# Optimization experiments

Measured on AMD Instinct MI355X. Metric: run time of the kernel, lower is better.

The kernel has to match this reference:

```python
import jax, jax.numpy as jnp
import numpy as np

B, S, D_MODEL, N_HEADS, D_K, D_V = 4, 1024, 1024, 16, 64, 64


def setup_inputs() -> dict:
    key = jax.random.key(0)
    ks = jax.random.split(key, 6)
    # xavier-normal std for [d_model, n_heads*d_k] weight
    std = float(np.sqrt(2.0 / (D_MODEL + N_HEADS * D_K)))
    return {
        "q": jax.random.normal(ks[0], (B, S, D_MODEL), jnp.float32),
        "k": jax.random.normal(ks[1], (B, S, D_MODEL), jnp.float32),
        "v": jax.random.normal(ks[2], (B, S, D_MODEL), jnp.float32),
        "w_q": jax.random.normal(ks[3], (D_MODEL, N_HEADS * D_K), jnp.float32) * std,
        "w_k": jax.random.normal(ks[4], (D_MODEL, N_HEADS * D_K), jnp.float32) * std,
        "w_v": jax.random.normal(ks[5], (D_MODEL, N_HEADS * D_V), jnp.float32) * std,
        "b_q": jnp.zeros((N_HEADS * D_K,), jnp.float32),
        "b_k": jnp.zeros((N_HEADS * D_K,), jnp.float32),
        "b_v": jnp.zeros((N_HEADS * D_V,), jnp.float32),
        "attn_mask": 0,  # falsy -> no masking, matching `if attn_mask:` in source
    }


def reference(q, k, v, w_q, w_k, w_v, b_q, b_k, b_v, attn_mask):
    b = q.shape[0]
    scale = jnp.sqrt(jnp.float32(D_K))
    # QKV projections -> [b, heads, seq, d]
    q_s = (q @ w_q + b_q).reshape(b, -1, N_HEADS, D_K).transpose(0, 2, 1, 3)
    k_s = (k @ w_k + b_k).reshape(b, -1, N_HEADS, D_K).transpose(0, 2, 1, 3)
    v_s = (v @ w_v + b_v).reshape(b, -1, N_HEADS, D_V).transpose(0, 2, 1, 3)
    scores = jnp.einsum("bhqd,bhkd->bhqk", q_s, k_s) / scale
    attn = jax.nn.softmax(scores, axis=-1)
    context = jnp.einsum("bhqk,bhkd->bhqd", attn, v_s)
    context = context.transpose(0, 2, 1, 3).reshape(b, -1, N_HEADS * D_V)
    return context, attn
```

## Files before the change

kernel.cpp:

```cpp
#include <hip/hip_runtime.h>

typedef unsigned short u16;
typedef __bf16 bf16x8 __attribute__((ext_vector_type(8)));
typedef float f32x4 __attribute__((ext_vector_type(4)));

__device__ __forceinline__ u16 f2b(float f) {
  unsigned u = __float_as_uint(f);
  return (u16)((u + 0x7FFFu + ((u >> 16) & 1u)) >> 16);
}
__device__ __forceinline__ float bl(unsigned w) { return __uint_as_float(w << 16); }
__device__ __forceinline__ float bh(unsigned w) { return __uint_as_float(w & 0xFFFF0000u); }

__device__ __forceinline__ void lds_load16(const void* g, void* l) {
  __builtin_amdgcn_global_load_lds(
      (__attribute__((address_space(1))) void*)(void*)g,
      (__attribute__((address_space(3))) void*)l, 16, 0, 0);
}

__global__ __launch_bounds__(256) void cvt_qkv(
    const float4* __restrict__ q, const float4* __restrict__ k, const float4* __restrict__ v,
    u16* __restrict__ qb, u16* __restrict__ kb, u16* __restrict__ vb) {
  int idx = blockIdx.x * 256 + threadIdx.x;
  int which = idx >> 20;
  int i = idx & 0xFFFFF;
  const float4* src = which == 0 ? q : which == 1 ? k : v;
  u16* dst = which == 0 ? qb : which == 1 ? kb : vb;
  float4 f = src[i];
  ushort4 o;
  o.x = f2b(f.x); o.y = f2b(f.y); o.z = f2b(f.z); o.w = f2b(f.w);
  *(ushort4*)(dst + (size_t)i * 4) = o;
}

__global__ __launch_bounds__(256) void transpose_cvt(
    const float* __restrict__ wq, const float* __restrict__ wk, const float* __restrict__ wv,
    u16* __restrict__ oq, u16* __restrict__ ok, u16* __restrict__ ov) {
  __shared__ float tile[32][33];
  int z = blockIdx.z;
  const float* in = z == 0 ? wq : z == 1 ? wk : wv;
  u16* out = z == 0 ? oq : z == 1 ? ok : ov;
  int x = blockIdx.x * 32 + threadIdx.x;
  for (int i = 0; i < 32; i += 8) {
    int y = blockIdx.y * 32 + threadIdx.y + i;
    tile[threadIdx.y + i][threadIdx.x] = in[(size_t)y * 1024 + x];
  }
  __syncthreads();
  int x2 = blockIdx.y * 32 + threadIdx.x;
  for (int i = 0; i < 32; i += 8) {
    int y2 = blockIdx.x * 32 + threadIdx.y + i;
    out[(size_t)y2 * 1024 + x2] = f2b(tile[threadIdx.x][threadIdx.y + i]);
  }
}

__global__ __launch_bounds__(256) void proj_gemm(
    const u16* __restrict__ qb, const u16* __restrict__ kb, const u16* __restrict__ vb,
    const u16* __restrict__ wqT, const u16* __restrict__ wkT, const u16* __restrict__ wvT,
    const float* __restrict__ bq, const float* __restrict__ bk, const float* __restrict__ bv,
    u16* __restrict__ q_s, u16* __restrict__ k_s, u16* __restrict__ vT_s) {
  __shared__ __align__(16) u16 As[128 * 64];
  __shared__ __align__(16) u16 Bs[128 * 64];
  const int z = blockIdx.z;
  const u16* A = z == 0 ? qb : z == 1 ? kb : vb;
  const u16* W = z == 0 ? wqT : z == 1 ? wkT : wvT;
  const float* bias = z == 0 ? bq : z == 1 ? bk : bv;

  const int t = threadIdx.x, lane = t & 63, wave = t >> 6;
  const int m0 = blockIdx.y * 128, n0 = blockIdx.x * 128;
  const int wm = (wave >> 1) * 64, wn = (wave & 1) * 64;

  f32x4 acc[4][4] = {};

  for (int k0 = 0; k0 < 1024; k0 += 64) {
    __syncthreads();
    #pragma unroll
    for (int r = 0; r < 4; ++r) {
      int flat = t + r * 256;
      int row = flat >> 3, gidx = (flat & 7) ^ (row & 7);
      lds_load16(A + (size_t)(m0 + row) * 1024 + k0 + gidx * 8, As + (size_t)flat * 8);
    }
    #pragma unroll
    for (int r = 0; r < 4; ++r) {
      int flat = t + r * 256;
      int row = flat >> 3, gidx = (flat & 7) ^ (row & 7);
      lds_load16(W + (size_t)(n0 + row) * 1024 + k0 + gidx * 8, Bs + (size_t)flat * 8);
    }
    __syncthreads();
    #pragma unroll
    for (int ks = 0; ks < 2; ++ks) {
      int kg = ks * 4 + (lane >> 4);
      bf16x8 af[4], bf[4];
      #pragma unroll
      for (int mi = 0; mi < 4; ++mi) {
        int rm = wm + mi * 16 + (lane & 15);
        af[mi] = *(const bf16x8*)(As + rm * 64 + ((kg ^ (rm & 7)) * 8));
      }
      #pragma unroll
      for (int ni = 0; ni < 4; ++ni) {
        int rn = wn + ni * 16 + (lane & 15);
        bf[ni] = *(const bf16x8*)(Bs + rn * 64 + ((kg ^ (rn & 7)) * 8));
      }
      #pragma unroll
      for (int mi = 0; mi < 4; ++mi)
        #pragma unroll
        for (int ni = 0; ni < 4; ++ni)
          acc[mi][ni] = __builtin_amdgcn_mfma_f32_16x16x32_bf16(af[mi], bf[ni], acc[mi][ni], 0, 0, 0);
    }
  }

  const float scale = (z == 0) ? 0.125f : 1.0f;
  #pragma unroll
  for (int mi = 0; mi < 4; ++mi) {
    #pragma unroll
    for (int ni = 0; ni < 4; ++ni) {
      int colb = n0 + wn + ni * 16 + (lane & 15);
      float bsv = bias[colb];
      int rowb0 = m0 + wm + mi * 16 + (lane >> 4) * 4;
      if (z == 2) {
        int bb = rowb0 >> 10, s0 = rowb0 & 1023;
        int hh = colb >> 6, dd = colb & 63;
        ushort4 o;
        o.x = f2b(acc[mi][ni][0] + bsv); o.y = f2b(acc[mi][ni][1] + bsv);
        o.z = f2b(acc[mi][ni][2] + bsv); o.w = f2b(acc[mi][ni][3] + bsv);
        *(ushort4*)(vT_s + ((((size_t)bb * 16 + hh) * 64 + dd) << 10) + s0) = o;
      } else {
        u16* dst = (z == 0) ? q_s : k_s;
        #pragma unroll
        for (int r = 0; r < 4; ++r)
          dst[(size_t)(rowb0 + r) * 1024 + colb] = f2b((acc[mi][ni][r] + bsv) * scale);
      }
    }
  }
}

#define SP_OFF   0
#define QT_OFF   132096
#define KV_OFF   140288
#define RED_OFF  156672
#define INV_OFF  158720
#define ATTN_LDS 158976

__global__ __launch_bounds__(512) void attn_kernel(
    const u16* __restrict__ q_s, const u16* __restrict__ k_s,
    const u16* __restrict__ vT_s, float* __restrict__ out_ctx,
    float* __restrict__ out_attn) {
  extern __shared__ __align__(16) char smem[];
  u16* s_p = (u16*)(smem + SP_OFF);
  u16* qt  = (u16*)(smem + QT_OFF);
  u16* kv  = (u16*)(smem + KV_OFF);
  float* red = (float*)(smem + RED_OFF);
  float* inv = (float*)(smem + INV_OFF);

  const int t = threadIdx.x, lane = t & 63, wave = t >> 6;
  const int mt = blockIdx.x, h = blockIdx.y, b = blockIdx.z;
  const int m0 = mt * 64;

  {
    int row = t >> 3, gidx = (t & 7) ^ (row & 7);
    lds_load16(q_s + ((size_t)(b * 1024 + m0 + row) * 1024 + h * 64 + gidx * 8),
               qt + (size_t)t * 8);
  }

  const int p1_mt = wave & 3;
  const int p1_nb = (wave >> 2) * 4;
  for (int c = 0; c < 8; ++c) {
    const int n0 = c * 128;
    __syncthreads();
    #pragma unroll
    for (int r = 0; r < 2; ++r) {
      int flat = t + r * 512;
      int row = flat >> 3, gidx = (flat & 7) ^ (row & 7);
      lds_load16(k_s + ((size_t)(b * 1024 + n0 + row) * 1024 + h * 64 + gidx * 8),
                 kv + (size_t)flat * 8);
    }
    __syncthreads();
    f32x4 acc[4] = {};
    #pragma unroll
    for (int ks = 0; ks < 2; ++ks) {
      int kg = ks * 4 + (lane >> 4);
      int am = p1_mt * 16 + (lane & 15);
      bf16x8 af = *(const bf16x8*)(qt + am * 64 + ((kg ^ (am & 7)) * 8));
      #pragma unroll
      for (int ni = 0; ni < 4; ++ni) {
        int bn = (p1_nb + ni) * 16 + (lane & 15);
        bf16x8 bf = *(const bf16x8*)(kv + bn * 64 + ((kg ^ (bn & 7)) * 8));
        acc[ni] = __builtin_amdgcn_mfma_f32_16x16x32_bf16(af, bf, acc[ni], 0, 0, 0);
      }
    }
    #pragma unroll
    for (int ni = 0; ni < 4; ++ni) {
      int col = n0 + (p1_nb + ni) * 16 + (lane & 15);
      int rbase = p1_mt * 16 + (lane >> 4) * 4;
      #pragma unroll
      for (int r = 0; r < 4; ++r) s_p[(rbase + r) * 1032 + col] = f2b(acc[ni][r]);
    }
  }

  __syncthreads();
  const int srow = t >> 3, sseg = t & 7;
  u16* rp = s_p + srow * 1032 + sseg * 128;
  float mx = -3.0e38f;
  #pragma unroll
  for (int i = 0; i < 16; ++i) {
    uint4 pk = *(const uint4*)(rp + i * 8);
    mx = fmaxf(mx, fmaxf(fmaxf(bl(pk.x), bh(pk.x)), fmaxf(bl(pk.y), bh(pk.y))));
    mx = fmaxf(mx, fmaxf(fmaxf(bl(pk.z), bh(pk.z)), fmaxf(bl(pk.w), bh(pk.w))));
  }
  red[t] = mx;
  __syncthreads();
  float rmx = red[srow * 8];
  #pragma unroll
  for (int j = 1; j < 8; ++j) rmx = fmaxf(rmx, red[srow * 8 + j]);
  __syncthreads();
  float sum = 0.f;
  #pragma unroll
  for (int i = 0; i < 16; ++i) {
    uint4 pk = *(const uint4*)(rp + i * 8);
    float e0 = __expf(bl(pk.x) - rmx), e1 = __expf(bh(pk.x) - rmx);
    float e2 = __expf(bl(pk.y) - rmx), e3 = __expf(bh(pk.y) - rmx);
    float e4 = __expf(bl(pk.z) - rmx), e5 = __expf(bh(pk.z) - rmx);
    float e6 = __expf(bl(pk.w) - rmx), e7 = __expf(bh(pk.w) - rmx);
    sum += ((e0 + e1) + (e2 + e3)) + ((e4 + e5) + (e6 + e7));
    pk.x = (unsigned)f2b(e0) | ((unsigned)f2b(e1) << 16);
    pk.y = (unsigned)f2b(e2) | ((unsigned)f2b(e3) << 16);
    pk.z = (unsigned)f2b(e4) | ((unsigned)f2b(e5) << 16);
    pk.w = (unsigned)f2b(e6) | ((unsigned)f2b(e7) << 16);
    *(uint4*)(rp + i * 8) = pk;
  }
  red[t] = sum;
  __syncthreads();
  float rs = 0.f;
  #pragma unroll
  for (int j = 0; j < 8; ++j) rs += red[srow * 8 + j];
  if (sseg == 0) inv[srow] = 1.0f / rs;
  __syncthreads();

  const size_t attn_base = ((size_t)(b * 16 + h) * 1024 + m0) << 10;
  #pragma unroll 4
  for (int it = 0; it < 32; ++it) {
    int flat = it * 512 + t;
    int r2 = flat >> 8, c4 = (flat & 255) << 2;
    float is = inv[r2];
    uint2 pk = *(const uint2*)(s_p + r2 * 1032 + c4);
    float4 o;
    o.x = bl(pk.x) * is; o.y = bh(pk.x) * is; o.z = bl(pk.y) * is; o.w = bh(pk.y) * is;
    *(float4*)(out_attn + attn_base + ((size_t)r2 << 10) + c4) = o;
  }

  const int p2_mt = wave >> 1;
  const int p2_nb = (wave & 1) * 2;
  f32x4 acc2[2] = {};
  for (int c = 0; c < 8; ++c) {
    const int j0 = c * 128;
    __syncthreads();
    #pragma unroll
    for (int r = 0; r < 2; ++r) {
      int flat = t + r * 512;
      int row = flat >> 4, gidx = (flat & 15) ^ (row & 15);
      lds_load16(vT_s + ((size_t)((b * 16 + h) * 64 + row) * 1024 + j0 + gidx * 8),
                 kv + (size_t)flat * 8);
    }
    __syncthreads();
    #pragma unroll
    for (int ks = 0; ks < 4; ++ks) {
      int kk = ks * 32 + (lane >> 4) * 8;
      int am = p2_mt * 16 + (lane & 15);
      bf16x8 af = *(const bf16x8*)(s_p + am * 1032 + j0 + kk);
      int kg = kk >> 3;
      #pragma unroll
      for (int ni = 0; ni < 2; ++ni) {
        int bn = (p2_nb + ni) * 16 + (lane & 15);
        bf16x8 bf = *(const bf16x8*)(kv + bn * 128 + ((kg ^ (bn & 15)) * 8));
        acc2[ni] = __builtin_amdgcn_mfma_f32_16x16x32_bf16(af, bf, acc2[ni], 0, 0, 0);
      }
    }
  }
  #pragma unroll
  for (int ni = 0; ni < 2; ++ni) {
    int col = (p2_nb + ni) * 16 + (lane & 15);
    int rbase = p2_mt * 16 + (lane >> 4) * 4;
    #pragma unroll
    for (int r = 0; r < 4; ++r) {
      int row = rbase + r;
      out_ctx[(size_t)(b * 1024 + m0 + row) * 1024 + h * 64 + col] = acc2[ni][r] * inv[row];
    }
  }
}

extern "C" void kernel_launch(void* const* d_in, const int* in_sizes, int n_in,
                              void* d_out, int out_size, void* d_ws, size_t ws_size,
                              hipStream_t stream) {
  const float* q  = (const float*)d_in[0];
  const float* k  = (const float*)d_in[1];
  const float* v  = (const float*)d_in[2];
  const float* wq = (const float*)d_in[3];
  const float* wk = (const float*)d_in[4];
  const float* wv = (const float*)d_in[5];
  const float* bq = (const float*)d_in[6];
  const float* bk = (const float*)d_in[7];
  const float* bv = (const float*)d_in[8];

  float* out_ctx  = (float*)d_out;
  float* out_attn = out_ctx + (size_t)4 * 1024 * 1024;

  u16* qb  = (u16*)d_ws;
  u16* kb  = qb  + (size_t)4194304;
  u16* vb  = kb  + (size_t)4194304;
  u16* wqT = vb  + (size_t)4194304;
  u16* wkT = wqT + (size_t)1048576;
  u16* wvT = wkT + (size_t)1048576;
  u16* q_s = wvT + (size_t)1048576;
  u16* k_s = q_s + (size_t)4194304;
  u16* vT  = k_s + (size_t)4194304;

  cvt_qkv<<<dim3(12288), 256, 0, stream>>>((const float4*)q, (const float4*)k,
                                           (const float4*)v, qb, kb, vb);
  transpose_cvt<<<dim3(32, 32, 3), dim3(32, 8), 0, stream>>>(wq, wk, wv, wqT, wkT, wvT);
  proj_gemm<<<dim3(8, 32, 3), 256, 0, stream>>>(qb, kb, vb, wqT, wkT, wvT,
                                                bq, bk, bv, q_s, k_s, vT);
  hipFuncSetAttribute((const void*)attn_kernel,
                      hipFuncAttributeMaxDynamicSharedMemorySize, ATTN_LDS);
  attn_kernel<<<dim3(16, 16, 4), 512, ATTN_LDS, stream>>>(q_s, k_s, vT, out_ctx, out_attn);
}
```

Before: 509.7 us.

## Recompute attention scores in two passes to shrink LDS and raise occupancy

The attention kernel no longer keeps a full 64x1024 bf16 score matrix in LDS. A first pass computes QK^T per 128-column chunk and accumulates row sums of exp(score) in registers. A second pass recomputes each chunk, exponentiates and normalises it, writes the attn output and feeds P·V directly. Max-subtraction is dropped, and shared memory falls from about 159KB to about 37KB, so several blocks can share a CU. The cost is a second QK^T pass and a risk of exp overflow when scores are large.

```diff
diff --git a/kernel.cpp b/kernel.cpp
--- a/kernel.cpp
+++ b/kernel.cpp
@@ -131,152 +131,145 @@
   }
 }
 
-#define SP_OFF   0
-#define QT_OFF   132096
-#define KV_OFF   140288
-#define RED_OFF  156672
-#define INV_OFF  158720
-#define ATTN_LDS 158976
-
-__global__ __launch_bounds__(512) void attn_kernel(
+__global__ __launch_bounds__(512, 6) void attn_kernel(
     const u16* __restrict__ q_s, const u16* __restrict__ k_s,
     const u16* __restrict__ vT_s, float* __restrict__ out_ctx,
     float* __restrict__ out_attn) {
-  extern __shared__ __align__(16) char smem[];
-  u16* s_p = (u16*)(smem + SP_OFF);
-  u16* qt  = (u16*)(smem + QT_OFF);
-  u16* kv  = (u16*)(smem + KV_OFF);
-  float* red = (float*)(smem + RED_OFF);
-  float* inv = (float*)(smem + INV_OFF);
+  __shared__ __align__(16) u16 qt[64 * 64];
+  __shared__ __align__(16) u16 kv[128 * 64];
+  __shared__ __align__(16) u16 sc[64 * 128];
+  __shared__ float red[8 * 64];
+  __shared__ float inv[64];
 
   const int t = threadIdx.x, lane = t & 63, wave = t >> 6;
-  const int mt = blockIdx.x, h = blockIdx.y, b = blockIdx.z;
-  const int m0 = mt * 64;
+  const int m0 = blockIdx.x * 64, h = blockIdx.y, b = blockIdx.z;
+  const int mt = wave & 3;
+  const int nh = wave >> 2;
+  const int l15 = lane & 15, lg = lane >> 4;
 
   {
-    int row = t >> 3, gidx = (t & 7) ^ (row & 7);
-    lds_load16(q_s + ((size_t)(b * 1024 + m0 + row) * 1024 + h * 64 + gidx * 8),
+    int row = t >> 3, g = t & 7;
+    lds_load16(q_s + ((size_t)(b * 1024 + m0 + row) * 1024 + h * 64 + ((g ^ (row & 7)) * 8)),
                qt + (size_t)t * 8);
   }
 
-  const int p1_mt = wave & 3;
-  const int p1_nb = (wave >> 2) * 4;
+  float sums[4] = {0.f, 0.f, 0.f, 0.f};
   for (int c = 0; c < 8; ++c) {
-    const int n0 = c * 128;
-    __syncthreads();
+    if (c) __syncthreads();
     #pragma unroll
     for (int r = 0; r < 2; ++r) {
       int flat = t + r * 512;
-      int row = flat >> 3, gidx = (flat & 7) ^ (row & 7);
-      lds_load16(k_s + ((size_t)(b * 1024 + n0 + row) * 1024 + h * 64 + gidx * 8),
+      int row = flat >> 3, g = flat & 7;
+      lds_load16(k_s + ((size_t)(b * 1024 + c * 128 + row) * 1024 + h * 64 + ((g ^ (row & 7)) * 8)),
                  kv + (size_t)flat * 8);
     }
     __syncthreads();
-    f32x4 acc[4] = {};
+    f32x4 a4[4] = {};
     #pragma unroll
     for (int ks = 0; ks < 2; ++ks) {
-      int kg = ks * 4 + (lane >> 4);
-      int am = p1_mt * 16 + (lane & 15);
+      int kg = ks * 4 + lg;
+      int am = mt * 16 + l15;
       bf16x8 af = *(const bf16x8*)(qt + am * 64 + ((kg ^ (am & 7)) * 8));
       #pragma unroll
       for (int ni = 0; ni < 4; ++ni) {
-        int bn = (p1_nb + ni) * 16 + (lane & 15);
+        int bn = (nh * 4 + ni) * 16 + l15;
         bf16x8 bf = *(const bf16x8*)(kv + bn * 64 + ((kg ^ (bn & 7)) * 8));
-        acc[ni] = __builtin_amdgcn_mfma_f32_16x16x32_bf16(af, bf, acc[ni], 0, 0, 0);
-      }
-    }
-    #pragma unroll
-    for (int ni = 0; ni < 4; ++ni) {
-      int col = n0 + (p1_nb + ni) * 16 + (lane & 15);
-      int rbase = p1_mt * 16 + (lane >> 4) * 4;
-      #pragma unroll
-      for (int r = 0; r < 4; ++r) s_p[(rbase + r) * 1032 + col] = f2b(acc[ni][r]);
-    }
-  }
-
+        a4[ni] = __builtin_amdgcn_mfma_f32_16x16x32_bf16(af, bf, a4[ni], 0, 0, 0);
+      }
+    }
+    #pragma unroll
+    for (int ni = 0; ni < 4; ++ni)
+      #pragma unroll
+      for (int r = 0; r < 4; ++r) sums[r] += __expf(a4[ni][r]);
+  }
+  #pragma unroll
+  for (int m = 1; m <= 8; m <<= 1)
+    #pragma unroll
+    for (int r = 0; r < 4; ++r) sums[r] += __shfl_xor(sums[r], m, 64);
+  if (l15 == 0) {
+    #pragma unroll
+    for (int r = 0; r < 4; ++r) red[wave * 64 + mt * 16 + lg * 4 + r] = sums[r];
+  }
   __syncthreads();
-  const int srow = t >> 3, sseg = t & 7;
-  u16* rp = s_p + srow * 1032 + sseg * 128;
-  float mx = -3.0e38f;
-  #pragma unroll
-  for (int i = 0; i < 16; ++i) {
-    uint4 pk = *(const uint4*)(rp + i * 8);
-    mx = fmaxf(mx, fmaxf(fmaxf(bl(pk.x), bh(pk.x)), fmaxf(bl(pk.y), bh(pk.y))));
-    mx = fmaxf(mx, fmaxf(fmaxf(bl(pk.z), bh(pk.z)), fmaxf(bl(pk.w), bh(pk.w))));
-  }
-  red[t] = mx;
-  __syncthreads();
-  float rmx = red[srow * 8];
-  #pragma unroll
-  for (int j = 1; j < 8; ++j) rmx = fmaxf(rmx, red[srow * 8 + j]);
-  __syncthreads();
-  float sum = 0.f;
-  #pragma unroll
-  for (int i = 0; i < 16; ++i) {
-    uint4 pk = *(const uint4*)(rp + i * 8);
-    float e0 = __expf(bl(pk.x) - rmx), e1 = __expf(bh(pk.x) - rmx);
-    float e2 = __expf(bl(pk.y) - rmx), e3 = __expf(bh(pk.y) - rmx);
-    float e4 = __expf(bl(pk.z) - rmx), e5 = __expf(bh(pk.z) - rmx);
-    float e6 = __expf(bl(pk.w) - rmx), e7 = __expf(bh(pk.w) - rmx);
-    sum += ((e0 + e1) + (e2 + e3)) + ((e4 + e5) + (e6 + e7));
-    pk.x = (unsigned)f2b(e0) | ((unsigned)f2b(e1) << 16);
-    pk.y = (unsigned)f2b(e2) | ((unsigned)f2b(e3) << 16);
-    pk.z = (unsigned)f2b(e4) | ((unsigned)f2b(e5) << 16);
-    pk.w = (unsigned)f2b(e6) | ((unsigned)f2b(e7) << 16);
-    *(uint4*)(rp + i * 8) = pk;
-  }
-  red[t] = sum;
-  __syncthreads();
-  float rs = 0.f;
-  #pragma unroll
-  for (int j = 0; j < 8; ++j) rs += red[srow * 8 + j];
-  if (sseg == 0) inv[srow] = 1.0f / rs;
-  __syncthreads();
-
-  const size_t attn_base = ((size_t)(b * 16 + h) * 1024 + m0) << 10;
-  #pragma unroll 4
-  for (int it = 0; it < 32; ++it) {
-    int flat = it * 512 + t;
-    int r2 = flat >> 8, c4 = (flat & 255) << 2;
-    float is = inv[r2];
-    uint2 pk = *(const uint2*)(s_p + r2 * 1032 + c4);
-    float4 o;
-    o.x = bl(pk.x) * is; o.y = bh(pk.x) * is; o.z = bl(pk.y) * is; o.w = bh(pk.y) * is;
-    *(float4*)(out_attn + attn_base + ((size_t)r2 << 10) + c4) = o;
-  }
-
-  const int p2_mt = wave >> 1;
-  const int p2_nb = (wave & 1) * 2;
+  if (t < 64) {
+    int w = t >> 4;
+    inv[t] = 1.0f / (red[w * 64 + t] + red[(w + 4) * 64 + t]);
+  }
+
+  const int qnp = (wave >> 2) * 2;
   f32x4 acc2[2] = {};
+  const size_t attn_row0 = ((size_t)(b * 16 + h) * 1024 + m0);
   for (int c = 0; c < 8; ++c) {
-    const int j0 = c * 128;
     __syncthreads();
     #pragma unroll
     for (int r = 0; r < 2; ++r) {
       int flat = t + r * 512;
-      int row = flat >> 4, gidx = (flat & 15) ^ (row & 15);
-      lds_load16(vT_s + ((size_t)((b * 16 + h) * 64 + row) * 1024 + j0 + gidx * 8),
+      int row = flat >> 3, g = flat & 7;
+      lds_load16(k_s + ((size_t)(b * 1024 + c * 128 + row) * 1024 + h * 64 + ((g ^ (row & 7)) * 8)),
                  kv + (size_t)flat * 8);
     }
     __syncthreads();
+    f32x4 a4[4] = {};
+    #pragma unroll
+    for (int ks = 0; ks < 2; ++ks) {
+      int kg = ks * 4 + lg;
+      int am = mt * 16 + l15;
+      bf16x8 af = *(const bf16x8*)(qt + am * 64 + ((kg ^ (am & 7)) * 8));
+      #pragma unroll
+      for (int ni = 0; ni < 4; ++ni) {
+        int bn = (nh * 4 + ni) * 16 + l15;
+        bf16x8 bf = *(const bf16x8*)(kv + bn * 64 + ((kg ^ (bn & 7)) * 8));
+        a4[ni] = __builtin_amdgcn_mfma_f32_16x16x32_bf16(af, bf, a4[ni], 0, 0, 0);
+      }
+    }
+    #pragma unroll
+    for (int ni = 0; ni < 4; ++ni) {
+      int col = (nh * 4 + ni) * 16 + l15;
+      int rbase = mt * 16 + lg * 4;
+      #pragma unroll
+      for (int r = 0; r < 4; ++r) {
+        int row = rbase + r;
+        sc[row * 128 + (((col >> 3) ^ (row & 15)) * 8) + (col & 7)] = f2b(__expf(a4[ni][r]));
+      }
+    }
+    __syncthreads();
+    #pragma unroll
+    for (int r = 0; r < 2; ++r) {
+      int flat = t + r * 512;
+      int row = flat >> 4, g = flat & 15;
+      lds_load16(vT_s + ((size_t)((b * 16 + h) * 64 + row) * 1024 + c * 128 + ((g ^ (row & 15)) * 8)),
+                 kv + (size_t)flat * 8);
+    }
+    {
+      #pragma unroll
+      for (int i = 0; i < 4; ++i) {
+        int flat = i * 512 + t;
+        int row = flat >> 5, c4 = (flat & 31) * 4;
+        float is = inv[row];
+        uint2 pk = *(const uint2*)(sc + row * 128 + (((c4 >> 3) ^ (row & 15)) * 8) + (c4 & 7));
+        float4 o;
+        o.x = bl(pk.x) * is; o.y = bh(pk.x) * is; o.z = bl(pk.y) * is; o.w = bh(pk.y) * is;
+        *(float4*)(out_attn + ((attn_row0 + row) << 10) + c * 128 + c4) = o;
+      }
+    }
+    __syncthreads();
     #pragma unroll
     for (int ks = 0; ks < 4; ++ks) {
-      int kk = ks * 32 + (lane >> 4) * 8;
-      int am = p2_mt * 16 + (lane & 15);
-      bf16x8 af = *(const bf16x8*)(s_p + am * 1032 + j0 + kk);
-      int kg = kk >> 3;
+      int kg = ks * 4 + lg;
+      int am = mt * 16 + l15;
+      bf16x8 af = *(const bf16x8*)(sc + am * 128 + ((kg ^ (am & 15)) * 8));
       #pragma unroll
       for (int ni = 0; ni < 2; ++ni) {
-        int bn = (p2_nb + ni) * 16 + (lane & 15);
-        bf16x8 bf = *(const bf16x8*)(kv + bn * 128 + ((kg ^ (bn & 15)) * 8));
+        int d = (qnp + ni) * 16 + l15;
+        bf16x8 bf = *(const bf16x8*)(kv + d * 128 + ((kg ^ (d & 15)) * 8));
         acc2[ni] = __builtin_amdgcn_mfma_f32_16x16x32_bf16(af, bf, acc2[ni], 0, 0, 0);
       }
     }
   }
   #pragma unroll
   for (int ni = 0; ni < 2; ++ni) {
-    int col = (p2_nb + ni) * 16 + (lane & 15);
-    int rbase = p2_mt * 16 + (lane >> 4) * 4;
+    int col = (qnp + ni) * 16 + l15;
+    int rbase = mt * 16 + lg * 4;
     #pragma unroll
     for (int r = 0; r < 4; ++r) {
       int row = rbase + r;
@@ -316,7 +309,5 @@
   transpose_cvt<<<dim3(32, 32, 3), dim3(32, 8), 0, stream>>>(wq, wk, wv, wqT, wkT, wvT);
   proj_gemm<<<dim3(8, 32, 3), 256, 0, stream>>>(qb, kb, vb, wqT, wkT, wvT,
                                                 bq, bk, bv, q_s, k_s, vT);
-  hipFuncSetAttribute((const void*)attn_kernel,
-                      hipFuncAttributeMaxDynamicSharedMemorySize, ATTN_LDS);
-  attn_kernel<<<dim3(16, 16, 4), 512, ATTN_LDS, stream>>>(q_s, k_s, vT, out_ctx, out_attn);
-}
+  attn_kernel<<<dim3(16, 16, 4), 512, 0, stream>>>(q_s, k_s, vT, out_ctx, out_attn);
+}
```

After: 477.3 us. 1.07x faster.
